# Performance work log

Measured on AMD Instinct MI355X. Metric: run time of the kernel, lower is better.

The kernel has to match this reference:

```python
import jax, jax.numpy as jnp
import numpy as np

K = 16          # neighbors used for attention (knn uses K+1 incl. self)
LRELU = 0.01    # torch LeakyReLU default negative_slope


def setup_inputs() -> dict:
    key = jax.random.key(0)
    ks = jax.random.split(key, 12)
    B, N = 4, 8192
    w = lambda k, shape: (jax.random.normal(k, shape, jnp.float32) * 0.05)
    inp = {
        "x": jax.random.normal(ks[0], (B, N, 3), jnp.float32),
        "global_feat": jax.random.normal(ks[1], (B, 1024), jnp.float32),  # unused by forward (matches source)
        # convs1 = MLP_CONV(3, [64,128]): Conv1d(3,64)+ReLU, Conv1d(64,128)
        "W1": w(ks[2], (64, 3)),    "b1": jnp.zeros((64,), jnp.float32),
        "W2": w(ks[3], (128, 64)),  "b2": jnp.zeros((128,), jnp.float32),
        # convs2: Conv2d(9,64,1x1)+LReLU, Conv2d(64,64,1x1)+LReLU, Conv2d(64,128,1x1)
        "Wc1": w(ks[4], (64, 9)),   "bc1": jnp.zeros((64,), jnp.float32),
        "Wc2": w(ks[5], (64, 64)),  "bc2": jnp.zeros((64,), jnp.float32),
        "Wc3": w(ks[6], (128, 64)), "bc3": jnp.zeros((128,), jnp.float32),
        # conv_query / conv_key: Conv2d(256,256,1x1)
        "Wq": w(ks[7], (256, 256)), "bq": jnp.zeros((256,), jnp.float32),
        "Wk": w(ks[8], (256, 256)), "bk": jnp.zeros((256,), jnp.float32),
    }
    return inp


def _lrelu(t):
    return jnp.where(t >= 0, t, LRELU * t)


def _forward(x, W1, b1, W2, b2, Wc1, bc1, Wc2, bc2, Wc3, bc3, Wq, bq, Wk, bk):
    # convs1: pointwise MLP on coords -> per-point features f [B,N,128]
    f = jax.nn.relu(jnp.einsum('bnc,oc->bno', x, W1) + b1)
    f = jnp.einsum('bnc,oc->bno', f, W2) + b2

    # knn_points(x, x, K=17): squared-distance matrix, nearest-first (self at slot 0)
    sq = jnp.sum(x * x, axis=-1)                              # [B,N]
    d2 = sq[:, :, None] + sq[:, None, :] - 2.0 * jnp.einsum('bnc,bmc->bnm', x, x)
    _, idx = jax.lax.top_k(-d2, K + 1)                        # [B,N,K+1]

    gather = jax.vmap(lambda a, i: a[i])                      # per-batch fancy gather
    knn_x = gather(x, idx)                                    # [B,N,K+1,3]
    knn_f = gather(f, idx)                                    # [B,N,K+1,128]

    rep = jnp.broadcast_to(x[:, :, None, :], knn_x.shape)     # repeat_x
    r = jnp.concatenate([rep, knn_x, rep - knn_x], axis=-1)   # [B,N,K+1,9]
    r = _lrelu(jnp.einsum('bnkc,oc->bnko', r, Wc1) + bc1)
    r = _lrelu(jnp.einsum('bnkc,oc->bnko', r, Wc2) + bc2)
    r = jnp.einsum('bnkc,oc->bnko', r, Wc3) + bc3             # [B,N,K+1,128]

    feat = jnp.concatenate([knn_f, r], axis=-1)               # [B,N,K+1,256]
    q = jnp.einsum('bnkc,oc->bnko', feat[:, :, :1, :], Wq) + bq   # [B,N,1,256]
    k = jnp.einsum('bnkc,oc->bnko', feat[:, :, 1:, :], Wk) + bk   # [B,N,K,256]
    w = jax.nn.softmax(jnp.sum(q * k, axis=-1), axis=-1)      # [B,N,K]
    new_x = jnp.sum(w[..., None] * knn_x[:, :, 1:, :], axis=2)    # [B,N,3]
    return new_x


def reference(x, global_feat, W1, b1, W2, b2, Wc1, bc1, Wc2, bc2, Wc3, bc3, Wq, bq, Wk, bk):
    del global_feat  # present in the torch signature but unused in forward
    return _forward(x, W1, b1, W2, b2, Wc1, bc1, Wc2, bc2, Wc3, bc3, Wq, bq, Wk, bk)
```

## Files before the change

kernel.cpp:

```cpp
#include <hip/hip_runtime.h>
#include <hip/hip_bf16.h>

#define NPTS 8192
#define NB   4

typedef unsigned short u16;
typedef unsigned int   u32;
typedef short bf16x8 __attribute__((ext_vector_type(8)));
typedef float f32x4  __attribute__((ext_vector_type(4)));

static __device__ __forceinline__ float bflo(u32 u){ return __uint_as_float(u << 16); }
static __device__ __forceinline__ float bfhi(u32 u){ return __uint_as_float(u & 0xffff0000u); }
static __device__ __forceinline__ u16 f2bf(float f){
  u32 x = __float_as_uint(f);
  return (u16)((x + 0x7fffu + ((x >> 16) & 1u)) >> 16);
}
static __device__ __forceinline__ float lrelu(float v){ return v >= 0.f ? v : 0.01f * v; }

__global__ __launch_bounds__(256) void k0_prep(const float* __restrict__ Wq, const float* __restrict__ bq,
                                               const float* __restrict__ Wk, const float* __restrict__ Wc3,
                                               const float* __restrict__ Wc2,
                                               u16* __restrict__ Mb, float* __restrict__ u,
                                               u16* __restrict__ Wc3T, u16* __restrict__ Wc2p){
  int oc = blockIdx.x, c = threadIdx.x;
  float acc = 0.f;
  for (int r = 0; r < 256; ++r) acc = fmaf(Wk[r*256 + oc], Wq[r*256 + c], acc);
  Mb[oc*256 + c] = f2bf(acc);
  __shared__ float red[256];
  red[c] = Wk[c*256 + oc] * bq[c];
  __syncthreads();
  for (int s = 128; s > 0; s >>= 1){ if (c < s) red[c] += red[c + s]; __syncthreads(); }
  if (c == 0) u[oc] = red[0];
  if (oc < 32){ int e = oc*256 + c; int h = e >> 7, o = e & 127; Wc3T[h*128 + o] = f2bf(Wc3[o*64 + h]); }
  if (oc >= 32 && oc < 48){ int e = (oc - 32)*256 + c; Wc2p[e] = f2bf(Wc2[e]); }
}

__global__ __launch_bounds__(128) void k1_feat(const float* __restrict__ x, const float* __restrict__ W1,
                                               const float* __restrict__ b1, const float* __restrict__ W2,
                                               const float* __restrict__ b2, u16* __restrict__ f){
  __shared__ float xs[16][4];
  __shared__ float hids[16][68];
  __shared__ float W2s[128][68];
  int b = blockIdx.y; int n0 = blockIdx.x * 16; int t = threadIdx.x;
  const float* xb = x + ((size_t)b*NPTS + n0)*3;
  if (t < 48){ int p = t/3, c = t - p*3; xs[p][c] = xb[p*3 + c]; }
  for (int e = t; e < 8192; e += 128) W2s[e >> 6][e & 63] = W2[e];
  __syncthreads();
  {
    int e = t;
    #pragma unroll
    for (int ii = 0; ii < 8; ++ii, e += 128){
      int p = e >> 6, h = e & 63;
      float v = b1[h];
      v = fmaf(W1[h*3+0], xs[p][0], v);
      v = fmaf(W1[h*3+1], xs[p][1], v);
      v = fmaf(W1[h*3+2], xs[p][2], v);
      hids[p][h] = v > 0.f ? v : 0.f;
    }
  }
  __syncthreads();
  int p = t >> 3, og = t & 7;
  float acc[16];
  #pragma unroll
  for (int i = 0; i < 16; ++i) acc[i] = b2[og + 8*i];
  #pragma unroll 4
  for (int c4 = 0; c4 < 16; ++c4){
    float4 hv = *(const float4*)&hids[p][c4*4];
    #pragma unroll
    for (int i = 0; i < 16; ++i){
      float4 wv = *(const float4*)&W2s[og + 8*i][c4*4];
      acc[i] = fmaf(wv.x, hv.x, acc[i]); acc[i] = fmaf(wv.y, hv.y, acc[i]);
      acc[i] = fmaf(wv.z, hv.z, acc[i]); acc[i] = fmaf(wv.w, hv.w, acc[i]);
    }
  }
  u16* fb = f + ((size_t)b*NPTS + n0)*128;
  #pragma unroll
  for (int i = 0; i < 16; ++i) fb[p*128 + og + 8*i] = f2bf(acc[i]);
}

#define K2_FLUSH8() do { \
    _Pragma("unroll") \
    for (int s = 0; s < 8; ++s){ \
      int2 pr = *(const int2*)(bufp + s*4096); \
      float d = (s < cnt) ? __int_as_float(pr.x) : __builtin_inff(); \
      int ii = pr.y; \
      bool pk = bd[11] > d; \
      _Pragma("unroll") \
      for (int k = 11; k >= 1; --k){ \
        bool pk1 = bd[k-1] > d; \
        float nd = pk1 ? bd[k-1] : d; \
        int   ni = pk1 ? bi[k-1] : ii; \
        if (pk){ bd[k] = nd; bi[k] = ni; } \
        pk = pk1; \
      } \
      if (pk){ bd[0] = d; bi[0] = ii; } \
    } \
    cnt = 0; } while (0)

__global__ __launch_bounds__(512) void k2_knn(const float* __restrict__ x, int* __restrict__ idxout){
#pragma clang fp contract(off)
  __shared__ __align__(16) char smem[43008];
  int t = threadIdx.x, lane = t & 63, w = t >> 6;
  int b = blockIdx.y;
  const float* xb = x + (size_t)b*NPTS*3;
  int q = blockIdx.x*64 + lane;
  float qx = xb[q*3+0], qy = xb[q*3+1], qz = xb[q*3+2];
  float qsq = (qx*qx + qy*qy) + qz*qz;
  float bd[12]; int bi[12];
  #pragma unroll
  for (int k = 0; k < 12; ++k){ bd[k] = __builtin_inff(); bi[k] = 0; }
  float4* tile = (float4*)smem;
  float*  tauv = (float*)(smem + 8192);
  char*   bufp = smem + 10240 + t*8;
  tauv[t] = __builtin_inff();
  __syncthreads();
  int cnt = 0;
  float gate = __builtin_inff();
  int c0 = w * 1024;
  for (int t0 = 0; t0 < 1024; t0 += 64){
    int m = c0 + t0 + lane;
    float cx = xb[m*3+0], cy = xb[m*3+1], cz = xb[m*3+2];
    float csq = (cx*cx + cy*cy) + cz*cz;
    tile[w*64 + lane] = make_float4(cx, cy, cz, csq);
    for (int j = 0; j < 64; ++j){
      float4 cd = tile[w*64 + j];
      float dt = (qx*cd.x + qy*cd.y) + qz*cd.z;
      float d2 = (qsq + cd.w) - 2.0f*dt;
      bool push = d2 < gate;
      if (__any(push)){
        if (push){
          *(int2*)(bufp + cnt*4096) = make_int2(__float_as_int(d2), c0 + t0 + j);
          ++cnt;
        }
        if (__any(cnt >= 8)){
          K2_FLUSH8();
          gate = fminf(gate, bd[11]);
        }
      }
    }
    tauv[t] = bd[11];
    float tm = fminf(tauv[lane], tauv[64 + lane]);
    tm = fminf(tm, fminf(tauv[128 + lane], tauv[192 + lane]));
    tm = fminf(tm, fminf(tauv[256 + lane], tauv[320 + lane]));
    tm = fminf(tm, fminf(tauv[384 + lane], tauv[448 + lane]));
    gate = fminf(tm, bd[11]);
  }
  K2_FLUSH8();
  __syncthreads();
  float* md   = (float*)smem;
  u16*   mi16 = (u16*)(smem + 24576);
  {
    int base = (w*64 + lane)*12;
    #pragma unroll
    for (int k = 0; k < 12; ++k){ md[base + k] = bd[k]; mi16[base + k] = (u16)bi[k]; }
  }
  __syncthreads();
  if (w == 0){
    const float inf = __builtin_inff();
    int p0=0,p1=0,p2=0,p3=0,p4=0,p5=0,p6=0,p7=0;
    int* op = idxout + ((size_t)b*NPTS + q)*17;
    int base = lane*12;
    for (int k = 0; k < 17; ++k){
      float h0 = (p0 < 12) ? md[       base + p0] : inf;
      float h1 = (p1 < 12) ? md[ 768 + base + p1] : inf;
      float h2 = (p2 < 12) ? md[1536 + base + p2] : inf;
      float h3 = (p3 < 12) ? md[2304 + base + p3] : inf;
      float h4 = (p4 < 12) ? md[3072 + base + p4] : inf;
      float h5 = (p5 < 12) ? md[3840 + base + p5] : inf;
      float h6 = (p6 < 12) ? md[4608 + base + p6] : inf;
      float h7 = (p7 < 12) ? md[5376 + base + p7] : inf;
      float best = h0; int ws = 0;
      if (h1 < best){ best = h1; ws = 1; }
      if (h2 < best){ best = h2; ws = 2; }
      if (h3 < best){ best = h3; ws = 3; }
      if (h4 < best){ best = h4; ws = 4; }
      if (h5 < best){ best = h5; ws = 5; }
      if (h6 < best){ best = h6; ws = 6; }
      if (h7 < best){ best = h7; ws = 7; }
      int pp = (ws==0)?p0:(ws==1)?p1:(ws==2)?p2:(ws==3)?p3:(ws==4)?p4:(ws==5)?p5:(ws==6)?p6:p7;
      op[k] = (int)mi16[ws*768 + base + pp];
      p0 += (ws==0); p1 += (ws==1); p2 += (ws==2); p3 += (ws==3);
      p4 += (ws==4); p5 += (ws==5); p6 += (ws==6); p7 += (ws==7);
    }
  }
}

__global__ __launch_bounds__(256) void k3_qt(const float* __restrict__ x, const int* __restrict__ idx,
    const u16* __restrict__ f, const u16* __restrict__ Mb, const float* __restrict__ u,
    const u16* __restrict__ Wc3T,
    const float* __restrict__ Wc1, const float* __restrict__ bc1,
    const float* __restrict__ Wc2, const float* __restrict__ bc2,
    const float* __restrict__ bc3, float* __restrict__ qg){
  __shared__ __align__(16) char smem[54016];
  u16*   featb = (u16*)smem;
  float* h1s   = (float*)(smem + 16896);
  float* h2s   = (float*)(smem + 25600);
  float* xgs   = (float*)(smem + 25600);
  int*   idx0s = (int*)(smem + 26112);
  float* qtBs  = (float*)(smem + 16896);
  float* xns   = (float*)(smem + 33792);
  float* Wc1s  = (float*)(smem + 34304);
  float* Wc2s  = (float*)(smem + 36608);
  u16*   W3s   = (u16*)(smem + 36608);

  int b = blockIdx.y; int n0 = blockIdx.x * 32; int t = threadIdx.x;
  const int p3 = t >> 3, hg = t & 7;

  if (t < 32) idx0s[t] = idx[((size_t)b*NPTS + n0 + t)*17];
  {
    const float* xb = x + ((size_t)b*NPTS + n0)*3;
    if (t < 96){ int p = t/3, c = t - p*3; xns[p*4 + c] = xb[p*3 + c]; }
  }
  for (int e = t; e < 576; e += 256) Wc1s[e] = Wc1[e];
  for (int e = t; e < 4096; e += 256) Wc2s[(e >> 6)*68 + (e & 63)] = Wc2[e];
  __syncthreads();
  if (t < 96){ int p = t/3, c = t - p*3; xgs[p*4 + c] = x[((size_t)b*NPTS + idx0s[p])*3 + c]; }
  {
    int cg = t & 7;
    const uint4* fsrc = (const uint4*)(f + ((size_t)b*NPTS + idx0s[p3])*128) + cg*2;
    uint4 A = fsrc[0], B = fsrc[1];
    uint4* dst = (uint4*)&featb[p3*264 + cg*16];
    dst[0] = A; dst[1] = B;
  }
  __syncthreads();
  {
    float rv0 = xns[p3*4+0], rv1 = xns[p3*4+1], rv2 = xns[p3*4+2];
    float rv3 = xgs[p3*4+0], rv4 = xgs[p3*4+1], rv5 = xgs[p3*4+2];
    float rv6 = rv0 - rv3, rv7 = rv1 - rv4, rv8 = rv2 - rv5;
    #pragma unroll
    for (int i = 0; i < 8; ++i){
      int h = hg + 8*i;
      const float* wr = &Wc1s[h*9];
      float v = bc1[h];
      v = fmaf(wr[0], rv0, v); v = fmaf(wr[1], rv1, v); v = fmaf(wr[2], rv2, v);
      v = fmaf(wr[3], rv3, v); v = fmaf(wr[4], rv4, v); v = fmaf(wr[5], rv5, v);
      v = fmaf(wr[6], rv6, v); v = fmaf(wr[7], rv7, v); v = fmaf(wr[8], rv8, v);
      h1s[p3*68 + h] = lrelu(v);
    }
  }
  __syncthreads();
  {
    #pragma unroll
    for (int i = 0; i < 8; ++i){
      int h = hg + 8*i;
      float v = bc2[h];
      const float* wr = &Wc2s[h*68];
      const float* ar = &h1s[p3*68];
      #pragma unroll
      for (int c4 = 0; c4 < 16; ++c4){
        float4 wv = *(const float4*)(wr + c4*4);
        float4 av = *(const float4*)(ar + c4*4);
        v = fmaf(wv.x, av.x, v); v = fmaf(wv.y, av.y, v);
        v = fmaf(wv.z, av.z, v); v = fmaf(wv.w, av.w, v);
      }
      h2s[p3*68 + h] = lrelu(v);
    }
  }
  __syncthreads();
  for (int e = t; e < 4096; e += 256) *(u32*)&W3s[(e >> 6)*136 + (e & 63)*2] = ((const u32*)Wc3T)[e];
  __syncthreads();
  {
    int og = hg;
    float4 a0 = *(const float4*)&bc3[og*16 + 0];
    float4 a1 = *(const float4*)&bc3[og*16 + 4];
    float4 a2 = *(const float4*)&bc3[og*16 + 8];
    float4 a3 = *(const float4*)&bc3[og*16 + 12];
    for (int h = 0; h < 64; ++h){
      float hv = h2s[p3*68 + h];
      const u32* wp = (const u32*)&W3s[h*136 + og*16];
      uint4 A = *(const uint4*)wp; uint4 B = *(const uint4*)(wp + 4);
      a0.x = fmaf(bflo(A.x), hv, a0.x); a0.y = fmaf(bfhi(A.x), hv, a0.y);
      a0.z = fmaf(bflo(A.y), hv, a0.z); a0.w = fmaf(bfhi(A.y), hv, a0.w);
      a1.x = fmaf(bflo(A.z), hv, a1.x); a1.y = fmaf(bfhi(A.z), hv, a1.y);
      a1.z = fmaf(bflo(A.w), hv, a1.z); a1.w = fmaf(bfhi(A.w), hv, a1.w);
      a2.x = fmaf(bflo(B.x), hv, a2.x); a2.y = fmaf(bfhi(B.x), hv, a2.y);
      a2.z = fmaf(bflo(B.y), hv, a2.z); a2.w = fmaf(bfhi(B.y), hv, a2.w);
      a3.x = fmaf(bflo(B.z), hv, a3.x); a3.y = fmaf(bfhi(B.z), hv, a3.y);
      a3.z = fmaf(bflo(B.w), hv, a3.z); a3.w = fmaf(bfhi(B.w), hv, a3.w);
    }
    u16* dst = &featb[p3*264 + 128 + og*16];
    u32 pw[8];
    pw[0] = (u32)f2bf(a0.x) | ((u32)f2bf(a0.y) << 16);
    pw[1] = (u32)f2bf(a0.z) | ((u32)f2bf(a0.w) << 16);
    pw[2] = (u32)f2bf(a1.x) | ((u32)f2bf(a1.y) << 16);
    pw[3] = (u32)f2bf(a1.z) | ((u32)f2bf(a1.w) << 16);
    pw[4] = (u32)f2bf(a2.x) | ((u32)f2bf(a2.y) << 16);
    pw[5] = (u32)f2bf(a2.z) | ((u32)f2bf(a2.w) << 16);
    pw[6] = (u32)f2bf(a3.x) | ((u32)f2bf(a3.y) << 16);
    pw[7] = (u32)f2bf(a3.z) | ((u32)f2bf(a3.w) << 16);
    ((uint4*)dst)[0] = make_uint4(pw[0], pw[1], pw[2], pw[3]);
    ((uint4*)dst)[1] = make_uint4(pw[4], pw[5], pw[6], pw[7]);
  }
  __syncthreads();
  {
    int lane = t & 63, wv = t >> 6;
    int l15 = lane & 15, kq = lane >> 4;
    f32x4 acc[2][4];
    #pragma unroll
    for (int rt = 0; rt < 2; ++rt)
      #pragma unroll
      for (int ct = 0; ct < 4; ++ct)
        acc[rt][ct] = (f32x4){0.f, 0.f, 0.f, 0.f};
    #pragma unroll
    for (int ks = 0; ks < 8; ++ks){
      bf16x8 a0 = *(const bf16x8*)&featb[l15*264 + ks*32 + kq*8];
      bf16x8 a1 = *(const bf16x8*)&featb[(16 + l15)*264 + ks*32 + kq*8];
      #pragma unroll
      for (int ct = 0; ct < 4; ++ct){
        int oc = wv*64 + ct*16 + l15;
        bf16x8 bb = *(const bf16x8*)(Mb + oc*256 + ks*32 + kq*8);
        acc[0][ct] = __builtin_amdgcn_mfma_f32_16x16x32_bf16(a0, bb, acc[0][ct], 0, 0, 0);
        acc[1][ct] = __builtin_amdgcn_mfma_f32_16x16x32_bf16(a1, bb, acc[1][ct], 0, 0, 0);
      }
    }
    if (wv < 2){
      float* qgb = qg + ((size_t)b*NPTS + n0)*192;
      #pragma unroll
      for (int ct = 0; ct < 4; ++ct){
        int oc = wv*64 + ct*16 + l15;
        float uv = u[oc];
        #pragma unroll
        for (int rt = 0; rt < 2; ++rt){
          #pragma unroll
          for (int j = 0; j < 4; ++j){
            int p = rt*16 + kq*4 + j;
            qgb[(size_t)p*192 + oc] = acc[rt][ct][j] + uv;
          }
        }
      }
    } else {
      #pragma unroll
      for (int ct = 0; ct < 4; ++ct){
        int oc = (wv - 2)*64 + ct*16 + l15;
        float uv = u[128 + oc];
        #pragma unroll
        for (int rt = 0; rt < 2; ++rt){
          #pragma unroll
          for (int j = 0; j < 4; ++j){
            int p = rt*16 + kq*4 + j;
            qtBs[p*132 + oc] = acc[rt][ct][j] + uv;
          }
        }
      }
    }
  }
  __syncthreads();
  {
    float gacc[8];
    #pragma unroll
    for (int i = 0; i < 8; ++i) gacc[i] = 0.f;
    for (int o8 = 0; o8 < 16; ++o8){
      const float* qr = &qtBs[p3*132 + o8*8];
      float4 qa = *(const float4*)qr; float4 qb4 = *(const float4*)(qr + 4);
      #pragma unroll
      for (int i = 0; i < 8; ++i){
        int h = hg + 8*i;
        const uint4 WU = *(const uint4*)&W3s[h*136 + o8*8];
        float acc = gacc[i];
        acc = fmaf(bflo(WU.x), qa.x, acc); acc = fmaf(bfhi(WU.x), qa.y, acc);
        acc = fmaf(bflo(WU.y), qa.z, acc); acc = fmaf(bfhi(WU.y), qa.w, acc);
        acc = fmaf(bflo(WU.z), qb4.x, acc); acc = fmaf(bfhi(WU.z), qb4.y, acc);
        acc = fmaf(bflo(WU.w), qb4.z, acc); acc = fmaf(bfhi(WU.w), qb4.w, acc);
        gacc[i] = acc;
      }
    }
    float* qgb = qg + ((size_t)b*NPTS + n0)*192;
    #pragma unroll
    for (int i = 0; i < 8; ++i) qgb[p3*192 + 128 + hg + 8*i] = gacc[i];
  }
}

__global__ __launch_bounds__(256) void k4_attn(const float* __restrict__ x, const int* __restrict__ idx,
    const u16* __restrict__ f, const float* __restrict__ qg,
    const float* __restrict__ Wc1, const float* __restrict__ bc1,
    const float* __restrict__ bc2, const u16* __restrict__ Wc2p,
    float* __restrict__ out){
  __shared__ int   idxs[16][17];
  __shared__ float xns[16][4];
  __shared__ float qgs[16][196];
  __shared__ float Wc1s[576];
  __shared__ float bcs[128];
  __shared__ float xjs[256][4];
  __shared__ float flog[256];
  __shared__ u16   h1t[256][76];
  int b = blockIdx.y; int n0 = blockIdx.x * 16; int t = threadIdx.x;
  for (int e = t; e < 272; e += 256){ int p = e/17, k = e - p*17; idxs[p][k] = idx[((size_t)b*NPTS + n0 + p)*17 + k]; }
  if (t < 48){ int p = t/3, c = t - p*3; xns[p][c] = x[((size_t)b*NPTS + n0 + p)*3 + c]; }
  if (t < 128) bcs[t] = (t < 64) ? bc1[t] : bc2[t - 64];
  for (int e = t; e < 576; e += 256) Wc1s[e] = Wc1[e];
  {
    const float* src = qg + ((size_t)b*NPTS + n0)*192;
    for (int e = t; e < 3072; e += 256){ int p = e/192, c = e - p*192; qgs[p][c] = src[e]; }
  }
  __syncthreads();
  {
    int p = t >> 4, j = t & 15;
    int nidx = idxs[p][j + 1];
    const float* xr = x + ((size_t)b*NPTS + nidx)*3;
    float cx = xr[0], cy = xr[1], cz = xr[2];
    *(float4*)&xjs[t][0] = make_float4(cx, cy, cz, 0.f);
    float rx = xns[p][0], ry = xns[p][1], rz = xns[p][2];
    float dx = rx - cx, dy = ry - cy, dz = rz - cz;
    float logit = 0.f;
    {
      const u32* fr = (const u32*)(f + ((size_t)b*NPTS + nidx)*128);
      #pragma unroll
      for (int c8 = 0; c8 < 16; ++c8){
        uint4 FU = *(const uint4*)(fr + c8*4);
        const float* qr = &qgs[p][c8*8];
        float4 qa = *(const float4*)qr; float4 qb4 = *(const float4*)(qr + 4);
        logit = fmaf(bflo(FU.x), qa.x, logit); logit = fmaf(bfhi(FU.x), qa.y, logit);
        logit = fmaf(bflo(FU.y), qa.z, logit); logit = fmaf(bfhi(FU.y), qa.w, logit);
        logit = fmaf(bflo(FU.z), qb4.x, logit); logit = fmaf(bfhi(FU.z), qb4.y, logit);
        logit = fmaf(bflo(FU.w), qb4.z, logit); logit = fmaf(bfhi(FU.w), qb4.w, logit);
      }
    }
    flog[t] = logit;
    float h1r[64];
    #pragma unroll
    for (int h = 0; h < 64; ++h){
      const float* wr = &Wc1s[h*9];
      float v = bcs[h];
      v = fmaf(wr[0], rx, v); v = fmaf(wr[1], ry, v); v = fmaf(wr[2], rz, v);
      v = fmaf(wr[3], cx, v); v = fmaf(wr[4], cy, v); v = fmaf(wr[5], cz, v);
      v = fmaf(wr[6], dx, v); v = fmaf(wr[7], dy, v); v = fmaf(wr[8], dz, v);
      h1r[h] = lrelu(v);
    }
    u16* hrow = &h1t[t][0];
    #pragma unroll
    for (int c8 = 0; c8 < 8; ++c8){
      u32 w0 = (u32)f2bf(h1r[c8*8+0]) | ((u32)f2bf(h1r[c8*8+1]) << 16);
      u32 w1 = (u32)f2bf(h1r[c8*8+2]) | ((u32)f2bf(h1r[c8*8+3]) << 16);
      u32 w2 = (u32)f2bf(h1r[c8*8+4]) | ((u32)f2bf(h1r[c8*8+5]) << 16);
      u32 w3 = (u32)f2bf(h1r[c8*8+6]) | ((u32)f2bf(h1r[c8*8+7]) << 16);
      *(uint4*)&hrow[c8*8] = make_uint4(w0, w1, w2, w3);
    }
  }
  __syncthreads();
  {
    int lane = t & 63, wv = t >> 6;
    int l15 = lane & 15, kq = lane >> 4;
    f32x4 acc[4][4];
    #pragma unroll
    for (int rt = 0; rt < 4; ++rt)
      #pragma unroll
      for (int ct = 0; ct < 4; ++ct)
        acc[rt][ct] = (f32x4){0.f, 0.f, 0.f, 0.f};
    #pragma unroll
    for (int ks = 0; ks < 2; ++ks){
      bf16x8 av[4];
      #pragma unroll
      for (int rt = 0; rt < 4; ++rt)
        av[rt] = *(const bf16x8*)&h1t[wv*64 + rt*16 + l15][ks*32 + kq*8];
      #pragma unroll
      for (int ct = 0; ct < 4; ++ct){
        bf16x8 bv = *(const bf16x8*)(Wc2p + (ct*16 + l15)*64 + ks*32 + kq*8);
        #pragma unroll
        for (int rt = 0; rt < 4; ++rt)
          acc[rt][ct] = __builtin_amdgcn_mfma_f32_16x16x32_bf16(av[rt], bv, acc[rt][ct], 0, 0, 0);
      }
    }
    float lg[4][4];
    #pragma unroll
    for (int rt = 0; rt < 4; ++rt)
      #pragma unroll
      for (int reg = 0; reg < 4; ++reg) lg[rt][reg] = 0.f;
    #pragma unroll
    for (int ct = 0; ct < 4; ++ct){
      int col = ct*16 + l15;
      float b2v = bcs[64 + col];
      #pragma unroll
      for (int rt = 0; rt < 4; ++rt){
        float gv = qgs[wv*4 + rt][128 + col];
        #pragma unroll
        for (int reg = 0; reg < 4; ++reg){
          float h2 = lrelu(acc[rt][ct][reg] + b2v);
          lg[rt][reg] = fmaf(gv, h2, lg[rt][reg]);
        }
      }
    }
    #pragma unroll
    for (int s = 1; s < 16; s <<= 1){
      #pragma unroll
      for (int rt = 0; rt < 4; ++rt)
        #pragma unroll
        for (int reg = 0; reg < 4; ++reg)
          lg[rt][reg] += __shfl_xor(lg[rt][reg], s, 64);
    }
    #pragma unroll
    for (int rt = 0; rt < 4; ++rt){
      float4 fl = *(const float4*)&flog[(wv*4 + rt)*16 + kq*4];
      float l0 = lg[rt][0] + fl.x, l1 = lg[rt][1] + fl.y;
      float l2 = lg[rt][2] + fl.z, l3 = lg[rt][3] + fl.w;
      float mx = fmaxf(fmaxf(l0, l1), fmaxf(l2, l3));
      mx = fmaxf(mx, __shfl_xor(mx, 16, 64));
      mx = fmaxf(mx, __shfl_xor(mx, 32, 64));
      float e0 = expf(l0 - mx), e1 = expf(l1 - mx), e2 = expf(l2 - mx), e3 = expf(l3 - mx);
      float sm = (e0 + e1) + (e2 + e3);
      sm += __shfl_xor(sm, 16, 64);
      sm += __shfl_xor(sm, 32, 64);
      int rbase = (wv*4 + rt)*16 + kq*4;
      float4 x0 = *(const float4*)&xjs[rbase + 0][0];
      float4 x1 = *(const float4*)&xjs[rbase + 1][0];
      float4 x2 = *(const float4*)&xjs[rbase + 2][0];
      float4 x3 = *(const float4*)&xjs[rbase + 3][0];
      float ox = e0*x0.x + e1*x1.x + e2*x2.x + e3*x3.x;
      float oy = e0*x0.y + e1*x1.y + e2*x2.y + e3*x3.y;
      float oz = e0*x0.z + e1*x1.z + e2*x2.z + e3*x3.z;
      ox += __shfl_xor(ox, 16, 64); ox += __shfl_xor(ox, 32, 64);
      oy += __shfl_xor(oy, 16, 64); oy += __shfl_xor(oy, 32, 64);
      oz += __shfl_xor(oz, 16, 64); oz += __shfl_xor(oz, 32, 64);
      if (kq == 0 && l15 == rt){
        float inv = 1.f / sm;
        float* op = out + ((size_t)b*NPTS + n0 + wv*4 + rt)*3;
        op[0] = ox * inv; op[1] = oy * inv; op[2] = oz * inv;
      }
    }
  }
}

extern "C" void kernel_launch(void* const* d_in, const int* in_sizes, int n_in,
                              void* d_out, int out_size, void* d_ws, size_t ws_size,
                              hipStream_t stream){
  (void)in_sizes; (void)n_in; (void)out_size; (void)ws_size;
  const float* x   = (const float*)d_in[0];
  const float* W1  = (const float*)d_in[2];
  const float* b1  = (const float*)d_in[3];
  const float* W2  = (const float*)d_in[4];
  const float* b2  = (const float*)d_in[5];
  const float* Wc1 = (const float*)d_in[6];
  const float* bc1 = (const float*)d_in[7];
  const float* Wc2 = (const float*)d_in[8];
  const float* bc2 = (const float*)d_in[9];
  const float* Wc3 = (const float*)d_in[10];
  const float* bc3 = (const float*)d_in[11];
  const float* Wq  = (const float*)d_in[12];
  const float* bq  = (const float*)d_in[13];
  const float* Wk  = (const float*)d_in[14];
  float* out = (float*)d_out;

  char* ws = (char*)d_ws;
  u16*   Mb   = (u16*)(ws + 0);
  float* u    = (float*)(ws + 131072);
  u16*   Wc3T = (u16*)(ws + 132096);
  u16*   Wc2p = (u16*)(ws + 153600);
  u16*   fbuf = (u16*)(ws + (1u << 20));
  int*   idxb = (int*)(ws + (16u << 20));
  float* qgb  = (float*)(ws + (32u << 20));

  k0_prep<<<dim3(256), dim3(256), 0, stream>>>(Wq, bq, Wk, Wc3, Wc2, Mb, u, Wc3T, Wc2p);
  k1_feat<<<dim3(512, NB), dim3(128), 0, stream>>>(x, W1, b1, W2, b2, fbuf);
  k2_knn<<<dim3(128, NB), dim3(512), 0, stream>>>(x, idxb);
  k3_qt<<<dim3(256, NB), dim3(256), 0, stream>>>(x, idxb, fbuf, Mb, u, Wc3T, Wc1, bc1, Wc2, bc2, bc3, qgb);
  k4_attn<<<dim3(512, NB), dim3(256), 0, stream>>>(x, idxb, fbuf, qgb, Wc1, bc1, bc2, Wc2p, out);
}
```

Measured before the change: 381.0 us.

## Split KNN candidate range across two blocks and merge partial top-17 lists

The KNN kernel now launches twice as many blocks, each scanning half of the candidate points (512 per wave instead of 1024) and writing a partial sorted top-17 list of distances and indices to workspace. A new merge kernel combines the two sorted lists per query into the final 17 indices. This raises the block count from 512 to 1024 to fill more compute units on the large GPU, at the cost of an extra launch, extra global traffic, and a weaker pruning gate because each block sees fewer candidates.

```diff
diff --git a/kernel.cpp b/kernel.cpp
--- a/kernel.cpp
+++ b/kernel.cpp
@@ -97,13 +97,16 @@
     } \
     cnt = 0; } while (0)
 
-__global__ __launch_bounds__(512) void k2_knn(const float* __restrict__ x, int* __restrict__ idxout){
+__global__ __launch_bounds__(512) void k2_knn(const float* __restrict__ x,
+                                              float* __restrict__ dbuf,
+                                              u16* __restrict__ ibuf){
 #pragma clang fp contract(off)
   __shared__ __align__(16) char smem[43008];
   int t = threadIdx.x, lane = t & 63, w = t >> 6;
   int b = blockIdx.y;
+  int qg64 = blockIdx.x >> 1, half = blockIdx.x & 1;
   const float* xb = x + (size_t)b*NPTS*3;
-  int q = blockIdx.x*64 + lane;
+  int q = qg64*64 + lane;
   float qx = xb[q*3+0], qy = xb[q*3+1], qz = xb[q*3+2];
   float qsq = (qx*qx + qy*qy) + qz*qz;
   float bd[12]; int bi[12];
@@ -116,8 +119,8 @@
   __syncthreads();
   int cnt = 0;
   float gate = __builtin_inff();
-  int c0 = w * 1024;
-  for (int t0 = 0; t0 < 1024; t0 += 64){
+  int c0 = half*4096 + w*512;
+  for (int t0 = 0; t0 < 512; t0 += 64){
     int m = c0 + t0 + lane;
     float cx = xb[m*3+0], cy = xb[m*3+1], cz = xb[m*3+2];
     float csq = (cx*cx + cy*cy) + cz*cz;
@@ -158,7 +161,9 @@
   if (w == 0){
     const float inf = __builtin_inff();
     int p0=0,p1=0,p2=0,p3=0,p4=0,p5=0,p6=0,p7=0;
-    int* op = idxout + ((size_t)b*NPTS + q)*17;
+    size_t obase = (((size_t)b*NPTS + q)*2 + half)*17;
+    float* od = dbuf + obase;
+    u16*   oi = ibuf + obase;
     int base = lane*12;
     for (int k = 0; k < 17; ++k){
       float h0 = (p0 < 12) ? md[       base + p0] : inf;
@@ -178,10 +183,35 @@
       if (h6 < best){ best = h6; ws = 6; }
       if (h7 < best){ best = h7; ws = 7; }
       int pp = (ws==0)?p0:(ws==1)?p1:(ws==2)?p2:(ws==3)?p3:(ws==4)?p4:(ws==5)?p5:(ws==6)?p6:p7;
-      op[k] = (int)mi16[ws*768 + base + pp];
+      od[k] = best;
+      oi[k] = mi16[ws*768 + base + pp];
       p0 += (ws==0); p1 += (ws==1); p2 += (ws==2); p3 += (ws==3);
       p4 += (ws==4); p5 += (ws==5); p6 += (ws==6); p7 += (ws==7);
     }
+  }
+}
+
+__global__ __launch_bounds__(256) void k2m_merge(const float* __restrict__ dbuf,
+                                                 const u16* __restrict__ ibuf,
+                                                 int* __restrict__ idxout){
+  int b = blockIdx.y;
+  int q = blockIdx.x*256 + threadIdx.x;
+  size_t base0 = (((size_t)b*NPTS + q)*2 + 0)*17;
+  size_t base1 = base0 + 17;
+  const float* D0 = dbuf + base0;
+  const float* D1 = dbuf + base1;
+  const u16*   I0 = ibuf + base0;
+  const u16*   I1 = ibuf + base1;
+  int* op = idxout + ((size_t)b*NPTS + q)*17;
+  const float inf = __builtin_inff();
+  int p0 = 0, p1 = 0;
+  #pragma unroll
+  for (int k = 0; k < 17; ++k){
+    float d0 = (p0 < 17) ? D0[p0] : inf;
+    float d1 = (p1 < 17) ? D1[p1] : inf;
+    bool take0 = d0 <= d1;
+    op[k] = take0 ? (int)I0[p0] : (int)I1[p1];
+    p0 += take0; p1 += !take0;
   }
 }
 
@@ -546,11 +576,14 @@
   u16*   Wc2p = (u16*)(ws + 153600);
   u16*   fbuf = (u16*)(ws + (1u << 20));
   int*   idxb = (int*)(ws + (16u << 20));
+  float* dbuf = (float*)(ws + (20u << 20));
+  u16*   ibuf = (u16*)(ws + (25u << 20));
   float* qgb  = (float*)(ws + (32u << 20));
 
   k0_prep<<<dim3(256), dim3(256), 0, stream>>>(Wq, bq, Wk, Wc3, Wc2, Mb, u, Wc3T, Wc2p);
   k1_feat<<<dim3(512, NB), dim3(128), 0, stream>>>(x, W1, b1, W2, b2, fbuf);
-  k2_knn<<<dim3(128, NB), dim3(512), 0, stream>>>(x, idxb);
+  k2_knn<<<dim3(256, NB), dim3(512), 0, stream>>>(x, dbuf, ibuf);
+  k2m_merge<<<dim3(32, NB), dim3(256), 0, stream>>>(dbuf, ibuf, idxb);
   k3_qt<<<dim3(256, NB), dim3(256), 0, stream>>>(x, idxb, fbuf, Mb, u, Wc3T, Wc1, bc1, Wc2, bc2, bc3, qgb);
   k4_attn<<<dim3(512, NB), dim3(256), 0, stream>>>(x, idxb, fbuf, qgb, Wc1, bc1, bc2, Wc2p, out);
 }
```

Result: slower. 401.4 us (+5.4%).
